# Optimization experiments

Hardware: AMD Instinct MI355X
Metric: run time of the kernel (lower is better)

Reference implementation:

```python
import jax, jax.numpy as jnp
import numpy as np

NUM_NODES = 20000
NUM_RELATIONS = 32
HIDDEN = 128
EMB = 16
NUM_EDGES = 600000


def setup_inputs() -> dict:
    key = jax.random.key(0)
    ks = jax.random.split(key, 8)
    edge_index = jax.random.randint(ks[0], (2, NUM_EDGES), 0, NUM_NODES, dtype=jnp.int64)
    edge_type = jax.random.randint(ks[1], (NUM_EDGES,), 0, NUM_RELATIONS, dtype=jnp.int64)
    node_emb = jax.random.normal(ks[2], (NUM_NODES, EMB), dtype=jnp.float32)
    W1 = jax.random.normal(ks[3], (NUM_RELATIONS, EMB, HIDDEN), dtype=jnp.float32) * (1.0 / np.sqrt(EMB))
    root1 = jax.random.normal(ks[4], (EMB, HIDDEN), dtype=jnp.float32) * (1.0 / np.sqrt(EMB))
    b1 = jnp.zeros((HIDDEN,), dtype=jnp.float32)
    W2 = jax.random.normal(ks[5], (NUM_RELATIONS, HIDDEN, HIDDEN), dtype=jnp.float32) * (1.0 / np.sqrt(HIDDEN))
    root2 = jax.random.normal(ks[6], (HIDDEN, HIDDEN), dtype=jnp.float32) * (1.0 / np.sqrt(HIDDEN))
    b2 = jnp.zeros((HIDDEN,), dtype=jnp.float32)
    return {"edge_index": edge_index, "edge_type": edge_type, "node_emb": node_emb,
            "W1": W1, "root1": root1, "b1": b1, "W2": W2, "root2": root2, "b2": b2}


def rgcn_layer(x, edge_index, edge_type, W, root, bias):
    # PyG RGCNConv: per-relation transform, per-(dst, relation) MEAN aggregation,
    # summed over relations, plus root transform and bias.
    src, dst = edge_index[0], edge_index[1]
    # mean normalization per (dst, relation) segment
    seg = dst * NUM_RELATIONS + edge_type                      # [E]
    counts = jax.ops.segment_sum(jnp.ones(seg.shape, jnp.float32), seg,
                                 num_segments=NUM_NODES * NUM_RELATIONS)
    inv = jnp.where(counts > 0, 1.0 / counts, 0.0)
    # transform every node by every relation weight: [N, R, H]
    xr = jnp.einsum('nf,rfh->nrh', x, W)
    msg = xr[src, edge_type] * inv[seg][:, None]               # [E, H]
    agg = jax.ops.segment_sum(msg, dst, num_segments=NUM_NODES)  # [N, H]
    return agg + x @ root + bias


def reference(edge_index, edge_type, node_emb, W1, root1, b1, W2, root2, b2):
    h = rgcn_layer(node_emb, edge_index, edge_type, W1, root1, b1)
    h = jax.nn.relu(h)
    h = rgcn_layer(h, edge_index, edge_type, W2, root2, b2)
    return h
```

## Files before the change

kernel.cpp:

```cpp
#include <hip/hip_runtime.h>
#include <hip/hip_bf16.h>

#define N_NODES 20000
#define N_REL 32
#define HID 128
#define EMB 16
#define N_EDGES 600000
#define NB (N_NODES * N_REL)

typedef __attribute__((ext_vector_type(8))) short  bf8v;
typedef __attribute__((ext_vector_type(8))) unsigned short us8v;
typedef __attribute__((ext_vector_type(4))) unsigned short us4v;
typedef __attribute__((ext_vector_type(4))) float  f4v;

__device__ __forceinline__ unsigned short f2b(float f) {
    __hip_bfloat16 h = __float2bfloat16(f);
    return __builtin_bit_cast(unsigned short, h);
}
__device__ __forceinline__ float b2f(unsigned short u) {
    unsigned int x = ((unsigned int)u) << 16;
    return __builtin_bit_cast(float, x);
}

__device__ __forceinline__ void lds_barrier() {
    asm volatile("s_waitcnt lgkmcnt(0)\n\ts_barrier" ::: "memory");
}

#define R_W2 (N_REL * HID * HID)
#define R_XB (N_NODES * 32)
#define R_W1 (N_REL * HID * 32)
#define R_R1 (HID * 32)
#define R_R2 (HID * HID)
#define R_HIST N_EDGES
#define PRE_TOT (R_W2 + R_XB + R_W1 + R_R1 + R_R2 + R_HIST)

__global__ __launch_bounds__(256) void pre1_k(
    const int* __restrict__ dst, const int* __restrict__ et,
    const float* __restrict__ x, const float* __restrict__ W1,
    const float* __restrict__ root1, const float* __restrict__ W2,
    const float* __restrict__ root2,
    int* __restrict__ hist,
    unsigned short* __restrict__ xb, unsigned short* __restrict__ w1t,
    unsigned short* __restrict__ r1t, unsigned short* __restrict__ w2t,
    unsigned short* __restrict__ r2t) {
    int i = blockIdx.x * 256 + threadIdx.x;
    if (i < R_W2) {
        int r = i >> 14, k = (i >> 7) & 127, n = i & 127;
        int ct8 = n >> 4, m16 = n & 15, ks = k >> 5, q = (k >> 3) & 3, j = k & 7;
        w2t[(size_t)r * 16384 + (ct8 * 4 + ks) * 512 + m16 * 32 + q * 8 + j] = f2b(W2[i]);
        return;
    }
    i -= R_W2;
    if (i < R_XB) {
        int n = i >> 5, k = i & 31;
        xb[i] = (k < EMB) ? f2b(x[n * EMB + k]) : (unsigned short)0;
        return;
    }
    i -= R_XB;
    if (i < R_W1) {
        int r = i >> 12, rem = i & 4095;
        int ct8 = rem >> 9, m16 = (rem >> 5) & 15, q = (rem >> 3) & 3, j = rem & 7;
        int n = ct8 * 16 + m16, k = q * 8 + j;
        w1t[i] = (k < EMB) ? f2b(W1[(r << 11) + (k << 7) + n]) : (unsigned short)0;
        return;
    }
    i -= R_W1;
    if (i < R_R1) {
        int ct8 = i >> 9, m16 = (i >> 5) & 15, q = (i >> 3) & 3, j = i & 7;
        int n = ct8 * 16 + m16, k = q * 8 + j;
        r1t[i] = (k < EMB) ? f2b(root1[(k << 7) + n]) : (unsigned short)0;
        return;
    }
    i -= R_R1;
    if (i < R_R2) {
        int ct8 = i >> 11, ks = (i >> 9) & 3, m16 = (i >> 5) & 15, q = (i >> 3) & 3, j = i & 7;
        int n = ct8 * 16 + m16, k = ks * 32 + q * 8 + j;
        r2t[i] = f2b(root2[(k << 7) + n]);
        return;
    }
    i -= R_R2;
    if (i < R_HIST) atomicAdd(&hist[dst[i] * N_REL + et[i]], 1);
}

__global__ void scan1_k(const int* __restrict__ hist, int* __restrict__ binoff,
                        int* __restrict__ bsum, float* __restrict__ inv) {
    __shared__ int sh[256];
    const int t = threadIdx.x;
    const int base = blockIdx.x * 1024 + t * 4;
    int4 h4 = *(const int4*)(hist + base);
    float4 iv4;
    iv4.x = h4.x > 0 ? 1.0f / h4.x : 0.0f;
    iv4.y = h4.y > 0 ? 1.0f / h4.y : 0.0f;
    iv4.z = h4.z > 0 ? 1.0f / h4.z : 0.0f;
    iv4.w = h4.w > 0 ? 1.0f / h4.w : 0.0f;
    *(float4*)(inv + base) = iv4;
    int ts = h4.x + h4.y + h4.z + h4.w;
    sh[t] = ts;
    __syncthreads();
    for (int o = 1; o < 256; o <<= 1) {
        int v = (t >= o) ? sh[t - o] : 0;
        __syncthreads();
        sh[t] += v;
        __syncthreads();
    }
    int exc = sh[t] - ts;
    binoff[base + 0] = exc;
    binoff[base + 1] = exc + h4.x;
    binoff[base + 2] = exc + h4.x + h4.y;
    binoff[base + 3] = exc + h4.x + h4.y + h4.z;
    if (t == 255) bsum[blockIdx.x] = sh[255];
}

__global__ void scan2_k(const int* __restrict__ bsum, int* __restrict__ bbase) {
    __shared__ int sh[1024];
    const int t = threadIdx.x;
    int v = (t < 625) ? bsum[t] : 0;
    sh[t] = v;
    __syncthreads();
    for (int o = 1; o < 1024; o <<= 1) {
        int u = (t >= o) ? sh[t - o] : 0;
        __syncthreads();
        sh[t] += u;
        __syncthreads();
    }
    if (t < 625) bbase[t] = sh[t] - v;
}

__global__ void scan3_k(int* __restrict__ binoff, const int* __restrict__ bbase,
                        int* __restrict__ cursors) {
    int i = blockIdx.x * 256 + threadIdx.x;
    if (i < NB) {
        int v = binoff[i] + bbase[i >> 10];
        binoff[i] = v;
        cursors[i] = v;
    }
    if (i == 0) binoff[NB] = N_EDGES;
}

__global__ void scatter_k(const int* __restrict__ src, const int* __restrict__ dst,
                          const int* __restrict__ et, int* __restrict__ cursors,
                          int* __restrict__ ssrc) {
    int e = blockIdx.x * 256 + threadIdx.x;
    if (e < 4) ssrc[N_EDGES + e] = 0;
    if (e < N_EDGES) {
        int b = dst[e] * N_REL + et[e];
        int p = atomicAdd(&cursors[b], 1);
        ssrc[p] = src[e];
    }
}

template<int KT, int LSS, int CW, int RG>
__global__ __launch_bounds__(256) void gemm_f(
    const int* __restrict__ binoff, const float* __restrict__ inv,
    const int* __restrict__ ssrc,
    const unsigned short* __restrict__ G,
    const unsigned short* __restrict__ Bw,
    const unsigned short* __restrict__ Br,
    float* __restrict__ part) {

    constexpr int ROW = KT * 32;
    constexpr int NCH = ROW / CW;
    constexpr int CP8 = CW / 8;
    static_assert(NCH * CW == ROW, "chunk covering must be exact");
    static_assert(32 * NCH <= 256, "one gather item per thread");

    __shared__ __align__(16) unsigned short As[2][32 * LSS];
    __shared__ int   smO[32 * (RG + 1)];
    __shared__ float smI[32 * RG];

    const int t = threadIdx.x;
    const int w = t >> 6, lane = t & 63;
    const int q = lane >> 4, m16 = lane & 15;
    const int d0 = blockIdx.x * 32;
    const int r0 = blockIdx.y * RG;
    const bool isLast = (blockIdx.y == gridDim.y - 1);
    const int colb = w * 32;
    const int cb16 = colb >> 4;
    const int fo = m16 * 32 + q * 8;
    const bool gat = t < 32 * NCH;
    const int grow = t / NCH, gcc = t % NCH;
    const int mb  = grow * (RG + 1);
    const int mbI = grow * RG;

    for (int i = t; i < 32 * (RG + 1); i += 256) {
        int row = i / (RG + 1), rr = i % (RG + 1);
        smO[i] = binoff[(d0 + row) * N_REL + r0 + rr];
    }
    for (int i = t; i < 32 * RG; i += 256) {
        int row = i / RG, rr = i % RG;
        smI[i] = inv[(d0 + row) * N_REL + r0 + rr];
    }
    lds_barrier();

    f4v acc[2][2];
#pragma unroll
    for (int rt = 0; rt < 2; ++rt)
#pragma unroll
        for (int ct = 0; ct < 2; ++ct) acc[rt][ct] = f4v{0.f, 0.f, 0.f, 0.f};

    us8v gE[4][CP8];
#pragma unroll
    for (int e = 0; e < 4; ++e)
#pragma unroll
        for (int j = 0; j < CP8; ++j) gE[e][j] = us8v{};
    int sx[4] = {0, 0, 0, 0};

    if (gat) {
        const int so = smO[mb], cnt = smO[mb + 1] - so;
        int s0 = ssrc[so], s1 = ssrc[so + 1], s2 = ssrc[so + 2], s3 = ssrc[so + 3];
        if (cnt >= 1) {
            const unsigned short* gp = G + (size_t)s0 * ROW + gcc * CW;
#pragma unroll
            for (int j = 0; j < CP8; ++j) gE[0][j] = *(const us8v*)(gp + j * 8);
        }
        if (cnt >= 2) {
            const unsigned short* gp = G + (size_t)s1 * ROW + gcc * CW;
#pragma unroll
            for (int j = 0; j < CP8; ++j) gE[1][j] = *(const us8v*)(gp + j * 8);
        }
        if (cnt >= 3) {
            const unsigned short* gp = G + (size_t)s2 * ROW + gcc * CW;
#pragma unroll
            for (int j = 0; j < CP8; ++j) gE[2][j] = *(const us8v*)(gp + j * 8);
        }
        if (cnt >= 4) {
            const unsigned short* gp = G + (size_t)s3 * ROW + gcc * CW;
#pragma unroll
            for (int j = 0; j < CP8; ++j) gE[3][j] = *(const us8v*)(gp + j * 8);
        }
        if (RG > 1) {
            const int so1 = smO[mb + 1];
            sx[0] = ssrc[so1]; sx[1] = ssrc[so1 + 1];
            sx[2] = ssrc[so1 + 2]; sx[3] = ssrc[so1 + 3];
        }
    }

    bf8v bfr[2][KT];
#pragma unroll
    for (int ct = 0; ct < 2; ++ct) {
#pragma unroll
        for (int ks = 0; ks < KT; ++ks)
            bfr[ct][ks] = *(const bf8v*)(Bw + (size_t)r0 * (HID * ROW)
                              + ((cb16 + ct) * KT + ks) * 512 + fo);
    }

    for (int it = 0; it < RG; ++it) {
        unsigned short* Ab = As[it & 1];
        if (gat) {
            const int so = smO[mb + it], eo = smO[mb + it + 1];
            const int cnt = eo - so;
            const float m2 = cnt >= 2 ? 1.f : 0.f;
            const float m3 = cnt >= 3 ? 1.f : 0.f;
            const float m4 = cnt >= 4 ? 1.f : 0.f;
            float a[CW];
#pragma unroll
            for (int j = 0; j < CP8; ++j)
#pragma unroll
                for (int k = 0; k < 8; ++k)
                    a[j * 8 + k] = b2f(gE[0][j][k]) + m2 * b2f(gE[1][j][k])
                                 + m3 * b2f(gE[2][j][k]) + m4 * b2f(gE[3][j][k]);
            for (int p = so + 4; p < eo; ++p) {
                const unsigned short* gp = G + (size_t)ssrc[p] * ROW + gcc * CW;
#pragma unroll
                for (int j = 0; j < CP8; ++j) {
                    us8v g = *(const us8v*)(gp + j * 8);
#pragma unroll
                    for (int k = 0; k < 8; ++k) a[j * 8 + k] += b2f(g[k]);
                }
            }
            const float iv = smI[mbI + it];
            unsigned short* wp = &Ab[grow * LSS + gcc * CW];
#pragma unroll
            for (int j = 0; j < CP8; ++j) {
                us8v sv;
#pragma unroll
                for (int k = 0; k < 8; ++k) sv[k] = f2b(a[j * 8 + k] * iv);
                *(us8v*)(wp + j * 8) = sv;
            }

            if (it + 1 < RG) {
                const int c1 = smO[mb + it + 2] - smO[mb + it + 1];
                if (c1 >= 1) {
                    const unsigned short* gp = G + (size_t)sx[0] * ROW + gcc * CW;
#pragma unroll
                    for (int j = 0; j < CP8; ++j) gE[0][j] = *(const us8v*)(gp + j * 8);
                }
                if (c1 >= 2) {
                    const unsigned short* gp = G + (size_t)sx[1] * ROW + gcc * CW;
#pragma unroll
                    for (int j = 0; j < CP8; ++j) gE[1][j] = *(const us8v*)(gp + j * 8);
                }
                if (c1 >= 3) {
                    const unsigned short* gp = G + (size_t)sx[2] * ROW + gcc * CW;
#pragma unroll
                    for (int j = 0; j < CP8; ++j) gE[2][j] = *(const us8v*)(gp + j * 8);
                }
                if (c1 >= 4) {
                    const unsigned short* gp = G + (size_t)sx[3] * ROW + gcc * CW;
#pragma unroll
                    for (int j = 0; j < CP8; ++j) gE[3][j] = *(const us8v*)(gp + j * 8);
                }
                if (it + 2 < RG) {
                    const int so2 = smO[mb + it + 2];
                    sx[0] = ssrc[so2]; sx[1] = ssrc[so2 + 1];
                    sx[2] = ssrc[so2 + 2]; sx[3] = ssrc[so2 + 3];
                }
            }
        }
        lds_barrier();

#pragma unroll
        for (int rt = 0; rt < 2; ++rt) {
            const unsigned short* ar = &Ab[(m16 + 16 * rt) * LSS];
#pragma unroll
            for (int ks = 0; ks < KT; ++ks) {
                bf8v af = *(const bf8v*)(ar + ks * 32 + q * 8);
                acc[rt][0] = __builtin_amdgcn_mfma_f32_16x16x32_bf16(af, bfr[0][ks], acc[rt][0], 0, 0, 0);
                acc[rt][1] = __builtin_amdgcn_mfma_f32_16x16x32_bf16(af, bfr[1][ks], acc[rt][1], 0, 0, 0);
            }
        }

        const unsigned short* Bp = (it + 1 < RG) ? (Bw + (size_t)(r0 + it + 1) * (HID * ROW))
                                                 : (isLast ? Br : nullptr);
        if (Bp) {
#pragma unroll
            for (int ct = 0; ct < 2; ++ct) {
#pragma unroll
                for (int ks = 0; ks < KT; ++ks)
                    bfr[ct][ks] = *(const bf8v*)(Bp + ((cb16 + ct) * KT + ks) * 512 + fo);
            }
        }
    }

    if (isLast) {
#pragma unroll
        for (int rt = 0; rt < 2; ++rt) {
#pragma unroll
            for (int ks = 0; ks < KT; ++ks) {
                bf8v af = *(const bf8v*)(G + (size_t)(d0 + m16 + 16 * rt) * ROW + ks * 32 + q * 8);
                acc[rt][0] = __builtin_amdgcn_mfma_f32_16x16x32_bf16(af, bfr[0][ks], acc[rt][0], 0, 0, 0);
                acc[rt][1] = __builtin_amdgcn_mfma_f32_16x16x32_bf16(af, bfr[1][ks], acc[rt][1], 0, 0, 0);
            }
        }
    }

    float* pb = part + (size_t)blockIdx.y * N_NODES * HID;
#pragma unroll
    for (int ct = 0; ct < 2; ++ct) {
        const int col = colb + 16 * ct + m16;
#pragma unroll
        for (int rt = 0; rt < 2; ++rt) {
#pragma unroll
            for (int g = 0; g < 4; ++g) {
                const int rr = 16 * rt + q * 4 + g;
                __builtin_nontemporal_store(acc[rt][ct][g],
                    &pb[(size_t)(d0 + rr) * HID + col]);
            }
        }
    }
}

__global__ __launch_bounds__(256) void reduce1_k(
    const float* __restrict__ part, const float* __restrict__ b1,
    unsigned short* __restrict__ h1b) {
    int i = blockIdx.x * 256 + threadIdx.x;
    if (i >= N_NODES * HID / 4) return;
    const size_t S = (size_t)N_NODES * HID;
    float4 bb = *(const float4*)(b1 + ((i * 4) & 127));
    float r0 = bb.x, r1 = bb.y, r2 = bb.z, r3 = bb.w;
#pragma unroll
    for (int p = 0; p < 2; ++p) {
        const float* pp = part + p * S + (size_t)i * 4;
        r0 += __builtin_nontemporal_load(pp + 0);
        r1 += __builtin_nontemporal_load(pp + 1);
        r2 += __builtin_nontemporal_load(pp + 2);
        r3 += __builtin_nontemporal_load(pp + 3);
    }
    us4v v;
    v[0] = f2b(fmaxf(r0, 0.0f));
    v[1] = f2b(fmaxf(r1, 0.0f));
    v[2] = f2b(fmaxf(r2, 0.0f));
    v[3] = f2b(fmaxf(r3, 0.0f));
    *(us4v*)(h1b + (size_t)i * 4) = v;
}

__global__ __launch_bounds__(256) void reduce2_k(
    const float* __restrict__ part, const float* __restrict__ b2,
    float* __restrict__ out) {
    int i = blockIdx.x * 256 + threadIdx.x;
    if (i >= N_NODES * HID / 4) return;
    const size_t S = (size_t)N_NODES * HID;
    float4 bb = *(const float4*)(b2 + ((i * 4) & 127));
    float r0 = bb.x, r1 = bb.y, r2 = bb.z, r3 = bb.w;
#pragma unroll
    for (int p = 0; p < 4; ++p) {
        const float* pp = part + p * S + (size_t)i * 4;
        r0 += __builtin_nontemporal_load(pp + 0);
        r1 += __builtin_nontemporal_load(pp + 1);
        r2 += __builtin_nontemporal_load(pp + 2);
        r3 += __builtin_nontemporal_load(pp + 3);
    }
    float4 r; r.x = r0; r.y = r1; r.z = r2; r.w = r3;
    ((float4*)out)[i] = r;
}

extern "C" void kernel_launch(void* const* d_in, const int* in_sizes, int n_in,
                              void* d_out, int out_size, void* d_ws, size_t ws_size,
                              hipStream_t stream) {
    const int*   ei    = (const int*)d_in[0];
    const int*   et    = (const int*)d_in[1];
    const float* x     = (const float*)d_in[2];
    const float* W1    = (const float*)d_in[3];
    const float* root1 = (const float*)d_in[4];
    const float* b1    = (const float*)d_in[5];
    const float* W2    = (const float*)d_in[6];
    const float* root2 = (const float*)d_in[7];
    const float* b2    = (const float*)d_in[8];
    float* out = (float*)d_out;

    char* ws = (char*)d_ws;
    size_t off = 0;
    auto alloc = [&](size_t bytes) { void* p = ws + off; off = (off + bytes + 63) & ~(size_t)63; return p; };
    int*   hist    = (int*)  alloc((size_t)NB * 4);
    int*   binoff  = (int*)  alloc((size_t)(NB + 1) * 4);
    int*   cursors = (int*)  alloc((size_t)NB * 4);
    float* inv     = (float*)alloc((size_t)NB * 4);
    int*   bsum    = (int*)  alloc(625 * 4);
    int*   bbase   = (int*)  alloc(625 * 4);
    int*   ssrc    = (int*)  alloc((size_t)(N_EDGES + 4) * 4);
    unsigned short* xb  = (unsigned short*)alloc((size_t)N_NODES * 32 * 2);
    unsigned short* h1b = (unsigned short*)alloc((size_t)N_NODES * HID * 2);
    unsigned short* w1t = (unsigned short*)alloc((size_t)N_REL * HID * 32 * 2);
    unsigned short* r1t = (unsigned short*)alloc((size_t)HID * 32 * 2);
    unsigned short* w2t = (unsigned short*)alloc((size_t)N_REL * HID * HID * 2);
    unsigned short* r2t = (unsigned short*)alloc((size_t)HID * HID * 2);
    float* part = (float*)alloc((size_t)4 * N_NODES * HID * 4);

    const int* src = ei;
    const int* dst = ei + N_EDGES;

    hipMemsetAsync(hist, 0, (size_t)NB * 4, stream);
    pre1_k<<<(PRE_TOT + 255) / 256, 256, 0, stream>>>(
        dst, et, x, W1, root1, W2, root2, hist, xb, w1t, r1t, w2t, r2t);
    scan1_k<<<NB / 1024, 256, 0, stream>>>(hist, binoff, bsum, inv);
    scan2_k<<<1, 1024, 0, stream>>>(bsum, bbase);
    scan3_k<<<(NB + 255) / 256, 256, 0, stream>>>(binoff, bbase, cursors);
    scatter_k<<<(N_EDGES + 255) / 256, 256, 0, stream>>>(src, dst, et, cursors, ssrc);

    gemm_f<1, 40, 8, 16><<<dim3(625, 2), 256, 0, stream>>>(
        binoff, inv, ssrc, xb, w1t, r1t, part);
    reduce1_k<<<(N_NODES * HID / 4 + 255) / 256, 256, 0, stream>>>(part, b1, h1b);

    gemm_f<4, 136, 16, 8><<<dim3(625, 4), 256, 0, stream>>>(
        binoff, inv, ssrc, h1b, w2t, r2t, part);
    reduce2_k<<<(N_NODES * HID / 4 + 255) / 256, 256, 0, stream>>>(part, b2, out);
}
```

Measured before the change: 246.5 us.

## Widen GEMM tiles to 64 destination rows with padded node count

Adds a row-tile template parameter so each GEMM block handles 64 destination nodes instead of 32, padding the node count to 20032 so it divides evenly, and sizes all bin/partial buffers and scans to match. Every thread now does one gather item (the idle-thread guard is gone), and layer 2 gathers 32-wide chunks per thread. The aim is to reuse each loaded weight fragment across more rows and use all threads for gathering, in exchange for more accumulator registers and fewer blocks. Padded rows depend on the pre-pass zeroing or handling the extra histogram and feature entries, which is not visible here.

```diff
diff --git a/kernel.cpp b/kernel.cpp
--- a/kernel.cpp
+++ b/kernel.cpp
@@ -2,11 +2,13 @@
 #include <hip/hip_bf16.h>
 
 #define N_NODES 20000
+#define NP 20032
 #define N_REL 32
 #define HID 128
 #define EMB 16
 #define N_EDGES 600000
 #define NB (N_NODES * N_REL)
+#define NBP (NP * N_REL)
 
 typedef __attribute__((ext_vector_type(8))) short  bf8v;
 typedef __attribute__((ext_vector_type(8))) unsigned short us8v;
@@ -114,7 +116,7 @@
 __global__ void scan2_k(const int* __restrict__ bsum, int* __restrict__ bbase) {
     __shared__ int sh[1024];
     const int t = threadIdx.x;
-    int v = (t < 625) ? bsum[t] : 0;
+    int v = (t < NBP / 1024) ? bsum[t] : 0;
     sh[t] = v;
     __syncthreads();
     for (int o = 1; o < 1024; o <<= 1) {
@@ -123,18 +125,18 @@
         sh[t] += u;
         __syncthreads();
     }
-    if (t < 625) bbase[t] = sh[t] - v;
+    if (t < NBP / 1024) bbase[t] = sh[t] - v;
 }
 
 __global__ void scan3_k(int* __restrict__ binoff, const int* __restrict__ bbase,
                         int* __restrict__ cursors) {
     int i = blockIdx.x * 256 + threadIdx.x;
-    if (i < NB) {
+    if (i < NBP) {
         int v = binoff[i] + bbase[i >> 10];
         binoff[i] = v;
         cursors[i] = v;
     }
-    if (i == 0) binoff[NB] = N_EDGES;
+    if (i == 0) binoff[NBP] = N_EDGES;
 }
 
 __global__ void scatter_k(const int* __restrict__ src, const int* __restrict__ dst,
@@ -149,7 +151,7 @@
     }
 }
 
-template<int KT, int LSS, int CW, int RG>
+template<int KT, int LSS, int CW, int RG, int RT>
 __global__ __launch_bounds__(256) void gemm_f(
     const int* __restrict__ binoff, const float* __restrict__ inv,
     const int* __restrict__ ssrc,
@@ -159,42 +161,42 @@
     float* __restrict__ part) {
 
     constexpr int ROW = KT * 32;
+    constexpr int NROWS = 16 * RT;
     constexpr int NCH = ROW / CW;
     constexpr int CP8 = CW / 8;
     static_assert(NCH * CW == ROW, "chunk covering must be exact");
-    static_assert(32 * NCH <= 256, "one gather item per thread");
-
-    __shared__ __align__(16) unsigned short As[2][32 * LSS];
-    __shared__ int   smO[32 * (RG + 1)];
-    __shared__ float smI[32 * RG];
+    static_assert(NROWS * NCH == 256, "one gather item per thread");
+
+    __shared__ __align__(16) unsigned short As[2][NROWS * LSS];
+    __shared__ int   smO[NROWS * (RG + 1)];
+    __shared__ float smI[NROWS * RG];
 
     const int t = threadIdx.x;
     const int w = t >> 6, lane = t & 63;
     const int q = lane >> 4, m16 = lane & 15;
-    const int d0 = blockIdx.x * 32;
+    const int d0 = blockIdx.x * NROWS;
     const int r0 = blockIdx.y * RG;
     const bool isLast = (blockIdx.y == gridDim.y - 1);
     const int colb = w * 32;
     const int cb16 = colb >> 4;
     const int fo = m16 * 32 + q * 8;
-    const bool gat = t < 32 * NCH;
     const int grow = t / NCH, gcc = t % NCH;
     const int mb  = grow * (RG + 1);
     const int mbI = grow * RG;
 
-    for (int i = t; i < 32 * (RG + 1); i += 256) {
+    for (int i = t; i < NROWS * (RG + 1); i += 256) {
         int row = i / (RG + 1), rr = i % (RG + 1);
         smO[i] = binoff[(d0 + row) * N_REL + r0 + rr];
     }
-    for (int i = t; i < 32 * RG; i += 256) {
+    for (int i = t; i < NROWS * RG; i += 256) {
         int row = i / RG, rr = i % RG;
         smI[i] = inv[(d0 + row) * N_REL + r0 + rr];
     }
     lds_barrier();
 
-    f4v acc[2][2];
-#pragma unroll
-    for (int rt = 0; rt < 2; ++rt)
+    f4v acc[RT][2];
+#pragma unroll
+    for (int rt = 0; rt < RT; ++rt)
 #pragma unroll
         for (int ct = 0; ct < 2; ++ct) acc[rt][ct] = f4v{0.f, 0.f, 0.f, 0.f};
 
@@ -205,7 +207,7 @@
         for (int j = 0; j < CP8; ++j) gE[e][j] = us8v{};
     int sx[4] = {0, 0, 0, 0};
 
-    if (gat) {
+    {
         const int so = smO[mb], cnt = smO[mb + 1] - so;
         int s0 = ssrc[so], s1 = ssrc[so + 1], s2 = ssrc[so + 2], s3 = ssrc[so + 3];
         if (cnt >= 1) {
@@ -246,7 +248,7 @@
 
     for (int it = 0; it < RG; ++it) {
         unsigned short* Ab = As[it & 1];
-        if (gat) {
+        {
             const int so = smO[mb + it], eo = smO[mb + it + 1];
             const int cnt = eo - so;
             const float m2 = cnt >= 2 ? 1.f : 0.f;
@@ -310,7 +312,7 @@
         lds_barrier();
 
 #pragma unroll
-        for (int rt = 0; rt < 2; ++rt) {
+        for (int rt = 0; rt < RT; ++rt) {
             const unsigned short* ar = &Ab[(m16 + 16 * rt) * LSS];
 #pragma unroll
             for (int ks = 0; ks < KT; ++ks) {
@@ -334,7 +336,7 @@
 
     if (isLast) {
 #pragma unroll
-        for (int rt = 0; rt < 2; ++rt) {
+        for (int rt = 0; rt < RT; ++rt) {
 #pragma unroll
             for (int ks = 0; ks < KT; ++ks) {
                 bf8v af = *(const bf8v*)(G + (size_t)(d0 + m16 + 16 * rt) * ROW + ks * 32 + q * 8);
@@ -344,12 +346,12 @@
         }
     }
 
-    float* pb = part + (size_t)blockIdx.y * N_NODES * HID;
+    float* pb = part + (size_t)blockIdx.y * NP * HID;
 #pragma unroll
     for (int ct = 0; ct < 2; ++ct) {
         const int col = colb + 16 * ct + m16;
 #pragma unroll
-        for (int rt = 0; rt < 2; ++rt) {
+        for (int rt = 0; rt < RT; ++rt) {
 #pragma unroll
             for (int g = 0; g < 4; ++g) {
                 const int rr = 16 * rt + q * 4 + g;
@@ -365,7 +367,7 @@
     unsigned short* __restrict__ h1b) {
     int i = blockIdx.x * 256 + threadIdx.x;
     if (i >= N_NODES * HID / 4) return;
-    const size_t S = (size_t)N_NODES * HID;
+    const size_t S = (size_t)NP * HID;
     float4 bb = *(const float4*)(b1 + ((i * 4) & 127));
     float r0 = bb.x, r1 = bb.y, r2 = bb.z, r3 = bb.w;
 #pragma unroll
@@ -389,7 +391,7 @@
     float* __restrict__ out) {
     int i = blockIdx.x * 256 + threadIdx.x;
     if (i >= N_NODES * HID / 4) return;
-    const size_t S = (size_t)N_NODES * HID;
+    const size_t S = (size_t)NP * HID;
     float4 bb = *(const float4*)(b2 + ((i * 4) & 127));
     float r0 = bb.x, r1 = bb.y, r2 = bb.z, r3 = bb.w;
 #pragma unroll
@@ -421,37 +423,37 @@
     char* ws = (char*)d_ws;
     size_t off = 0;
     auto alloc = [&](size_t bytes) { void* p = ws + off; off = (off + bytes + 63) & ~(size_t)63; return p; };
-    int*   hist    = (int*)  alloc((size_t)NB * 4);
-    int*   binoff  = (int*)  alloc((size_t)(NB + 1) * 4);
-    int*   cursors = (int*)  alloc((size_t)NB * 4);
-    float* inv     = (float*)alloc((size_t)NB * 4);
-    int*   bsum    = (int*)  alloc(625 * 4);
-    int*   bbase   = (int*)  alloc(625 * 4);
+    int*   hist    = (int*)  alloc((size_t)NBP * 4);
+    int*   binoff  = (int*)  alloc((size_t)(NBP + 1) * 4);
+    int*   cursors = (int*)  alloc((size_t)NBP * 4);
+    float* inv     = (float*)alloc((size_t)NBP * 4);
+    int*   bsum    = (int*)  alloc((NBP / 1024) * 4);
+    int*   bbase   = (int*)  alloc((NBP / 1024) * 4);
     int*   ssrc    = (int*)  alloc((size_t)(N_EDGES + 4) * 4);
-    unsigned short* xb  = (unsigned short*)alloc((size_t)N_NODES * 32 * 2);
-    unsigned short* h1b = (unsigned short*)alloc((size_t)N_NODES * HID * 2);
+    unsigned short* xb  = (unsigned short*)alloc((size_t)NP * 32 * 2);
+    unsigned short* h1b = (unsigned short*)alloc((size_t)NP * HID * 2);
     unsigned short* w1t = (unsigned short*)alloc((size_t)N_REL * HID * 32 * 2);
     unsigned short* r1t = (unsigned short*)alloc((size_t)HID * 32 * 2);
     unsigned short* w2t = (unsigned short*)alloc((size_t)N_REL * HID * HID * 2);
     unsigned short* r2t = (unsigned short*)alloc((size_t)HID * HID * 2);
-    float* part = (float*)alloc((size_t)4 * N_NODES * HID * 4);
+    float* part = (float*)alloc((size_t)4 * NP * HID * 4);
 
     const int* src = ei;
     const int* dst = ei + N_EDGES;
 
-    hipMemsetAsync(hist, 0, (size_t)NB * 4, stream);
+    hipMemsetAsync(hist, 0, (size_t)NBP * 4, stream);
     pre1_k<<<(PRE_TOT + 255) / 256, 256, 0, stream>>>(
         dst, et, x, W1, root1, W2, root2, hist, xb, w1t, r1t, w2t, r2t);
-    scan1_k<<<NB / 1024, 256, 0, stream>>>(hist, binoff, bsum, inv);
+    scan1_k<<<NBP / 1024, 256, 0, stream>>>(hist, binoff, bsum, inv);
     scan2_k<<<1, 1024, 0, stream>>>(bsum, bbase);
-    scan3_k<<<(NB + 255) / 256, 256, 0, stream>>>(binoff, bbase, cursors);
+    scan3_k<<<(NBP + 255) / 256, 256, 0, stream>>>(binoff, bbase, cursors);
     scatter_k<<<(N_EDGES + 255) / 256, 256, 0, stream>>>(src, dst, et, cursors, ssrc);
 
-    gemm_f<1, 40, 8, 16><<<dim3(625, 2), 256, 0, stream>>>(
+    gemm_f<1, 40, 8, 16, 4><<<dim3(NP / 64, 2), 256, 0, stream>>>(
         binoff, inv, ssrc, xb, w1t, r1t, part);
     reduce1_k<<<(N_NODES * HID / 4 + 255) / 256, 256, 0, stream>>>(part, b1, h1b);
 
-    gemm_f<4, 136, 16, 8><<<dim3(625, 4), 256, 0, stream>>>(
+    gemm_f<4, 136, 32, 8, 4><<<dim3(NP / 64, 4), 256, 0, stream>>>(
         binoff, inv, ssrc, h1b, w2t, r2t, part);
     reduce2_k<<<(N_NODES * HID / 4 + 255) / 256, 256, 0, stream>>>(part, b2, out);
 }
```

Result: slower. 251.8 us (+2.1%).
